# Performance work log

Hardware: AMD Instinct MI355X
Metric: run time of the kernel (lower is better)

The kernel has to match this reference:

```python
import jax, jax.numpy as jnp
import numpy as np
import math

# dims
C2, C1, T = 32, 64, 2048      # x shape
AVGF = 32                     # num_submatrices
SEG = T // AVGF               # 64
M = C1 * C2                   # M_size1 = 2048
TK = 3                        # num_blocks
HA = 16                       # num_heads
DH = M // HA                  # 128
EPS = 1e-5


def setup_inputs() -> dict:
    key = jax.random.key(0)
    ks = jax.random.split(key, 12)
    sc = 0.02  # scale params to keep fp32 activations finite
    return {
        "x": jax.random.normal(ks[0], (C2, C1, T), dtype=jnp.float32),
        "weight": jax.random.normal(ks[1], (M, M), dtype=jnp.float32) * sc,
        "Wqkv": jax.random.normal(ks[2], (TK, 3, HA, DH, M), dtype=jnp.float32) * sc,
        "Wo": jax.random.normal(ks[3], (TK, M, M), dtype=jnp.float32) * sc,
        "ln1_g": jnp.ones((M,), jnp.float32),
        "ln1_b": jnp.zeros((M,), jnp.float32),
        "ln2_g": jnp.ones((M,), jnp.float32),
        "ln2_b": jnp.zeros((M,), jnp.float32),
        "fc1_w": jax.random.normal(ks[4], (4 * M, M), dtype=jnp.float32) * sc,
        "fc1_b": jnp.zeros((4 * M,), jnp.float32),
        "fc2_w": jax.random.normal(ks[5], (M, 4 * M), dtype=jnp.float32) * sc,
        "fc2_b": jnp.zeros((M,), jnp.float32),
    }


def _ln(x, g, b):
    mu = jnp.mean(x, axis=-1, keepdims=True)
    var = jnp.var(x, axis=-1, keepdims=True)
    return (x - mu) / jnp.sqrt(var + EPS) * g + b


def _sinusoidal_bias():
    # bias[i, 2j]   = sin(i / 10000**(2*(2j)/M))  -- exponent uses even column index
    # bias[i, 2j+1] = cos(same angle)
    i = jnp.arange(AVGF, dtype=jnp.float32)[:, None]          # [avgf, 1]
    j = jnp.arange(0, M, 2, dtype=jnp.float32)[None, :]       # [1, M/2] even cols
    ang = i / jnp.power(10000.0, 2.0 * j / M)                 # [avgf, M/2]
    return jnp.stack([jnp.sin(ang), jnp.cos(ang)], axis=-1).reshape(AVGF, M)


def reference(x, weight, Wqkv, Wo, ln1_g, ln1_b, ln2_g, ln2_b,
              fc1_w, fc1_b, fc2_w, fc2_b):
    inp = jnp.transpose(x, (2, 1, 0))                          # [T, C1, C2]
    # segment-average over time -> [avgf, C1, C2]
    inputc = inp.reshape(AVGF, SEG, C1, C2).mean(axis=1)
    altx = inputc.reshape(AVGF, M)                             # [avgf, M]
    s = jnp.einsum('lm,im->il', weight, altx)                  # [avgf, M]
    s = s + _sinusoidal_bias()
    inv_sqrt_dh = 1.0 / math.sqrt(DH)
    for a in range(TK):                                        # fixed small block loop
        y = _ln(s, ln1_g, ln1_b)
        qkv = jnp.einsum('xhdm,im->xihd', Wqkv[a], y)          # [3, avgf, hA, Dh]
        q, k, v = qkv[0], qkv[1], qkv[2]
        rsa = jnp.einsum('ihd,ihd->ih', q * inv_sqrt_dh, k)    # per-token scalar attn
        imv = jnp.cumsum(rsa[..., None] * v, axis=0)           # serial inter-block scan
        s = jnp.einsum('nm,im->in', Wo[a], imv.reshape(AVGF, M)) + s
        s = _ln(s, ln2_g, ln2_b) + s
        h = jax.nn.gelu(s @ fc1_w.T + fc1_b, approximate=False)
        s = h @ fc2_w.T + fc2_b
    return s.reshape(AVGF, C1, C2)
```

## Files before the change

kernel.cpp:

```cpp
#include <hip/hip_runtime.h>
#include <math.h>

typedef __attribute__((ext_vector_type(4))) float f32x4;
typedef __attribute__((ext_vector_type(8))) short bf16x8;

__device__ inline short f2bf(float f) {
    union { float f; unsigned u; } v; v.f = f;
    unsigned u = v.u;
    u += 0x7fffu + ((u >> 16) & 1u);
    return (short)(u >> 16);
}

__global__ __launch_bounds__(256) void k_avg_init(const float* __restrict__ x,
                                                  float* __restrict__ altx,
                                                  float* __restrict__ s) {
    int blk = blockIdx.x, t = threadIdx.x;
    if (blk < 512) {
        int wv = t >> 6, lane = t & 63;
        int p = blk * 4 + wv;
        const float* row = x + (size_t)p * 2048;
        int c2 = p >> 6, c1 = p & 63;
        int m = c1 * 32 + c2;
        for (int seg = 0; seg < 32; ++seg) {
            float v = row[seg * 64 + lane];
            for (int off = 32; off; off >>= 1) v += __shfl_xor(v, off, 64);
            if (lane == 0) altx[seg * 2048 + m] = v * (1.0f / 64.0f);
        }
    } else {
        int i = blk - 512;
        const float kln = logf(10000.0f) / 1024.0f;
        for (int l = t; l < 2048; l += 256) {
            int c = l & ~1;
            float ang = (float)i * expf(-(float)c * kln);
            s[i * 2048 + l] = (l & 1) ? cosf(ang) : sinf(ang);
        }
    }
}

__device__ inline void row_stats(const float* __restrict__ row, float& mu, float& rstd) {
    float sm = 0.f, ss = 0.f;
    for (int idx = threadIdx.x; idx < 2048; idx += 256) {
        float v = row[idx]; sm += v; ss += v * v;
    }
    for (int off = 32; off; off >>= 1) {
        sm += __shfl_xor(sm, off, 64);
        ss += __shfl_xor(ss, off, 64);
    }
    __shared__ float as[4], bs[4];
    int wv = threadIdx.x >> 6, lane = threadIdx.x & 63;
    if (lane == 0) { as[wv] = sm; bs[wv] = ss; }
    __syncthreads();
    sm = as[0] + as[1] + as[2] + as[3];
    ss = bs[0] + bs[1] + bs[2] + bs[3];
    mu = sm * (1.0f / 2048.0f);
    float var = ss * (1.0f / 2048.0f) - mu * mu;
    rstd = rsqrtf(var + 1e-5f);
}

__global__ __launch_bounds__(256) void k_prep1(const float* __restrict__ s,
                                               const float* __restrict__ g,
                                               const float* __restrict__ b,
                                               float* __restrict__ y,
                                               float* __restrict__ s2,
                                               float* __restrict__ qkv) {
    int blk = blockIdx.x;
    if (blk < 32) {
        const float* row = s + blk * 2048;
        float mu, rstd; row_stats(row, mu, rstd);
        float* yr = y + blk * 2048;
        float* cr = s2 + blk * 2048;
        for (int idx = threadIdx.x; idx < 2048; idx += 256) {
            float v = row[idx];
            yr[idx] = (v - mu) * rstd * g[idx] + b[idx];
            cr[idx] = v;
        }
    } else {
        int z = blk - 32;
        float4* p4 = (float4*)(qkv + (size_t)z * 8192);
        float4 zero = {0.f, 0.f, 0.f, 0.f};
        for (int idx = threadIdx.x; idx < 2048; idx += 256) p4[idx] = zero;
    }
}

__global__ __launch_bounds__(256) void k_scan(const float* __restrict__ qkv,
                                              float* __restrict__ imv) {
    int h = blockIdx.x, t = threadIdx.x;
    __shared__ float rsa[32];
    if (t < 32) {
        const float* qr = qkv + (size_t)t * 6144 + h * 128;
        const float* kr = qr + 2048;
        float acc = 0.f;
        for (int d = 0; d < 128; ++d) acc += qr[d] * kr[d];
        rsa[t] = acc * 0.08838834764831845f;
    }
    __syncthreads();
    if (t < 128) {
        float acc = 0.f;
        for (int i = 0; i < 32; ++i) {
            acc += rsa[i] * qkv[(size_t)i * 6144 + 4096 + h * 128 + t];
            imv[i * 2048 + h * 128 + t] = acc;
        }
    }
}

__global__ __launch_bounds__(256) void k_prep2(const float* __restrict__ s2,
                                               const float* __restrict__ g,
                                               const float* __restrict__ b,
                                               float* __restrict__ sout,
                                               float* __restrict__ h) {
    int blk = blockIdx.x;
    if (blk < 32) {
        const float* row = s2 + blk * 2048;
        float mu, rstd; row_stats(row, mu, rstd);
        float* sr = sout + blk * 2048;
        for (int idx = threadIdx.x; idx < 2048; idx += 256) {
            float v = row[idx];
            sr[idx] = (v - mu) * rstd * g[idx] + b[idx] + v;
        }
    } else {
        int z = blk - 32;
        float4* p4 = (float4*)(h + (size_t)z * 8192);
        float4 zero = {0.f, 0.f, 0.f, 0.f};
        for (int idx = threadIdx.x; idx < 2048; idx += 256) p4[idx] = zero;
    }
}

__global__ __launch_bounds__(256) void k_act(float* __restrict__ h,
                                             const float* __restrict__ fc1_b,
                                             float* __restrict__ sout,
                                             const float* __restrict__ fc2_b) {
    int blk = blockIdx.x, t = threadIdx.x;
    if (blk < 128) {
        size_t base = ((size_t)blk * 256 + t) * 8;
        #pragma unroll
        for (int j = 0; j < 8; ++j) {
            size_t idx = base + j;
            float v = h[idx] + fc1_b[idx & 8191];
            h[idx] = 0.5f * v * (1.0f + erff(v * 0.70710678118654752f));
        }
    } else {
        size_t base = ((size_t)(blk - 128) * 256 + t) * 8;
        #pragma unroll
        for (int j = 0; j < 8; ++j) {
            size_t idx = base + j;
            sout[idx] = fc2_b[idx & 2047];
        }
    }
}

template<int TAG>
__global__ __launch_bounds__(256, 4) void k_gemm(const float* __restrict__ W,
                                                 const float* __restrict__ act,
                                                 float* __restrict__ out,
                                                 int N, int K) {
    constexpr int KC = 128;
    constexpr int S = KC / 32;
    __shared__ short lAs[32][KC + 8];
    int t = threadIdx.x;
    int lane = t & 63, wv = t >> 6;
    int m = lane & 15, q = lane >> 4;
    int nb = blockIdx.x * 64 + wv * 16;
    size_t kbeg = (size_t)blockIdx.y * KC;

    constexpr int APT = KC / 8;
    int arow = t >> 3, acol = (t & 7) * APT;
    const float* ap = act + (size_t)arow * K + kbeg + acol;
    float4 areg[APT / 4];
    #pragma unroll
    for (int j = 0; j < APT / 4; ++j) areg[j] = *(const float4*)(ap + j * 4);

    const float* B = W + (size_t)(nb + m) * K + kbeg + q * 8;
    float4 Bb[2 * S];
    #pragma unroll
    for (int s = 0; s < S; ++s) {
        Bb[2 * s]     = *(const float4*)(B + s * 32);
        Bb[2 * s + 1] = *(const float4*)(B + s * 32 + 4);
    }

    #pragma unroll
    for (int j = 0; j < APT / 4; ++j) {
        short4 c = { f2bf(areg[j].x), f2bf(areg[j].y), f2bf(areg[j].z), f2bf(areg[j].w) };
        *(short4*)&lAs[arow][acol + j * 4] = c;
    }
    __syncthreads();

    f32x4 acc0 = {0.f,0.f,0.f,0.f};
    f32x4 acc1 = {0.f,0.f,0.f,0.f};
    #pragma unroll
    for (int s = 0; s < S; ++s) {
        bf16x8 fa0 = *(const bf16x8*)&lAs[m][s * 32 + q * 8];
        bf16x8 fa1 = *(const bf16x8*)&lAs[m + 16][s * 32 + q * 8];
        float4 bl = Bb[2 * s], bh = Bb[2 * s + 1];
        bf16x8 fb = { f2bf(bl.x), f2bf(bl.y), f2bf(bl.z), f2bf(bl.w),
                      f2bf(bh.x), f2bf(bh.y), f2bf(bh.z), f2bf(bh.w) };
        acc0 = __builtin_amdgcn_mfma_f32_16x16x32_bf16(fa0, fb, acc0, 0, 0, 0);
        acc1 = __builtin_amdgcn_mfma_f32_16x16x32_bf16(fa1, fb, acc1, 0, 0, 0);
    }

    float* op = out + (size_t)(q * 4) * N + nb + m;
    #pragma unroll
    for (int r = 0; r < 4; ++r) {
        atomicAdd(op + (size_t)r * N, acc0[r]);
        atomicAdd(op + (size_t)(r + 16) * N, acc1[r]);
    }
}

extern "C" void kernel_launch(void* const* d_in, const int* in_sizes, int n_in,
                              void* d_out, int out_size, void* d_ws, size_t ws_size,
                              hipStream_t stream) {
    const float* x      = (const float*)d_in[0];
    const float* weight = (const float*)d_in[1];
    const float* Wqkv   = (const float*)d_in[2];
    const float* Wo     = (const float*)d_in[3];
    const float* ln1_g  = (const float*)d_in[4];
    const float* ln1_b  = (const float*)d_in[5];
    const float* ln2_g  = (const float*)d_in[6];
    const float* ln2_b  = (const float*)d_in[7];
    const float* fc1_w  = (const float*)d_in[8];
    const float* fc1_b  = (const float*)d_in[9];
    const float* fc2_w  = (const float*)d_in[10];
    const float* fc2_b  = (const float*)d_in[11];
    float* ws   = (float*)d_ws;
    float* altx = ws;
    float* sbuf = ws + 65536;
    float* y    = ws + 131072;
    float* s2   = ws + 196608;
    float* imv  = ws + 262144;
    float* qkv  = ws + 327680;
    float* h    = ws + 524288;
    float* outF = (float*)d_out;

    k_avg_init<<<544, 256, 0, stream>>>(x, altx, sbuf);
    k_gemm<0><<<dim3(32, 16), 256, 0, stream>>>(weight, altx, sbuf, 2048, 2048);
    for (int a = 0; a < 3; ++a) {
        k_prep1<<<56, 256, 0, stream>>>(sbuf, ln1_g, ln1_b, y, s2, qkv);
        k_gemm<1><<<dim3(96, 16), 256, 0, stream>>>(Wqkv + (size_t)a * 12582912, y, qkv, 6144, 2048);
        k_scan<<<16, 256, 0, stream>>>(qkv, imv);
        k_gemm<2><<<dim3(32, 16), 256, 0, stream>>>(Wo + (size_t)a * 4194304, imv, s2, 2048, 2048);
        k_prep2<<<64, 256, 0, stream>>>(s2, ln2_g, ln2_b, sbuf, h);
        k_gemm<3><<<dim3(128, 16), 256, 0, stream>>>(fc1_w, sbuf, h, 8192, 2048);
        float* sout = (a == 2) ? outF : sbuf;
        k_act<<<160, 256, 0, stream>>>(h, fc1_b, sout, fc2_b);
        k_gemm<4><<<dim3(32, 64), 256, 0, stream>>>(fc2_w, h, sout, 2048, 8192);
    }
}
```

Measured before the change: 552.5 us.

## Replace atomic split-K accumulation with partial buffers reduced in consumer kernels

The GEMM kernel now writes per-split partial results to a scratch pool with plain stores instead of atomicAdd. Downstream kernels (layernorm, scan, GELU, final output) sum the partials, so the separate zeroing and bias-init passes disappear. Each block also covers a larger K range (256 or 512) and double-buffers its weight register loads, which means fewer splits and less partial traffic. The costs are extra scratch memory, partial-sum reads in every consumer, and higher register use, reflected in the lower launch-bounds occupancy hint.

```diff
diff --git a/kernel.cpp b/kernel.cpp
--- a/kernel.cpp
+++ b/kernel.cpp
@@ -13,7 +13,7 @@
 
 __global__ __launch_bounds__(256) void k_avg_init(const float* __restrict__ x,
                                                   float* __restrict__ altx,
-                                                  float* __restrict__ s) {
+                                                  float* __restrict__ bias0) {
     int blk = blockIdx.x, t = threadIdx.x;
     if (blk < 512) {
         int wv = t >> 6, lane = t & 63;
@@ -32,176 +32,215 @@
         for (int l = t; l < 2048; l += 256) {
             int c = l & ~1;
             float ang = (float)i * expf(-(float)c * kln);
-            s[i * 2048 + l] = (l & 1) ? cosf(ang) : sinf(ang);
-        }
-    }
-}
-
-__device__ inline void row_stats(const float* __restrict__ row, float& mu, float& rstd) {
-    float sm = 0.f, ss = 0.f;
-    for (int idx = threadIdx.x; idx < 2048; idx += 256) {
-        float v = row[idx]; sm += v; ss += v * v;
-    }
-    for (int off = 32; off; off >>= 1) {
-        sm += __shfl_xor(sm, off, 64);
-        ss += __shfl_xor(ss, off, 64);
-    }
-    __shared__ float as[4], bs[4];
-    int wv = threadIdx.x >> 6, lane = threadIdx.x & 63;
-    if (lane == 0) { as[wv] = sm; bs[wv] = ss; }
-    __syncthreads();
-    sm = as[0] + as[1] + as[2] + as[3];
-    ss = bs[0] + bs[1] + bs[2] + bs[3];
-    mu = sm * (1.0f / 2048.0f);
-    float var = ss * (1.0f / 2048.0f) - mu * mu;
-    rstd = rsqrtf(var + 1e-5f);
-}
-
-__global__ __launch_bounds__(256) void k_prep1(const float* __restrict__ s,
-                                               const float* __restrict__ g,
-                                               const float* __restrict__ b,
-                                               float* __restrict__ y,
-                                               float* __restrict__ s2,
-                                               float* __restrict__ qkv) {
-    int blk = blockIdx.x;
-    if (blk < 32) {
-        const float* row = s + blk * 2048;
-        float mu, rstd; row_stats(row, mu, rstd);
-        float* yr = y + blk * 2048;
-        float* cr = s2 + blk * 2048;
-        for (int idx = threadIdx.x; idx < 2048; idx += 256) {
-            float v = row[idx];
-            yr[idx] = (v - mu) * rstd * g[idx] + b[idx];
-            cr[idx] = v;
-        }
-    } else {
-        int z = blk - 32;
-        float4* p4 = (float4*)(qkv + (size_t)z * 8192);
-        float4 zero = {0.f, 0.f, 0.f, 0.f};
-        for (int idx = threadIdx.x; idx < 2048; idx += 256) p4[idx] = zero;
-    }
-}
-
-__global__ __launch_bounds__(256) void k_scan(const float* __restrict__ qkv,
-                                              float* __restrict__ imv) {
-    int h = blockIdx.x, t = threadIdx.x;
-    __shared__ float rsa[32];
-    if (t < 32) {
-        const float* qr = qkv + (size_t)t * 6144 + h * 128;
-        const float* kr = qr + 2048;
-        float acc = 0.f;
-        for (int d = 0; d < 128; ++d) acc += qr[d] * kr[d];
-        rsa[t] = acc * 0.08838834764831845f;
-    }
-    __syncthreads();
-    if (t < 128) {
-        float acc = 0.f;
-        for (int i = 0; i < 32; ++i) {
-            acc += rsa[i] * qkv[(size_t)i * 6144 + 4096 + h * 128 + t];
-            imv[i * 2048 + h * 128 + t] = acc;
-        }
-    }
-}
-
-__global__ __launch_bounds__(256) void k_prep2(const float* __restrict__ s2,
-                                               const float* __restrict__ g,
-                                               const float* __restrict__ b,
-                                               float* __restrict__ sout,
-                                               float* __restrict__ h) {
-    int blk = blockIdx.x;
-    if (blk < 32) {
-        const float* row = s2 + blk * 2048;
-        float mu, rstd; row_stats(row, mu, rstd);
-        float* sr = sout + blk * 2048;
-        for (int idx = threadIdx.x; idx < 2048; idx += 256) {
-            float v = row[idx];
-            sr[idx] = (v - mu) * rstd * g[idx] + b[idx] + v;
-        }
-    } else {
-        int z = blk - 32;
-        float4* p4 = (float4*)(h + (size_t)z * 8192);
-        float4 zero = {0.f, 0.f, 0.f, 0.f};
-        for (int idx = threadIdx.x; idx < 2048; idx += 256) p4[idx] = zero;
-    }
-}
-
-__global__ __launch_bounds__(256) void k_act(float* __restrict__ h,
-                                             const float* __restrict__ fc1_b,
-                                             float* __restrict__ sout,
-                                             const float* __restrict__ fc2_b) {
-    int blk = blockIdx.x, t = threadIdx.x;
-    if (blk < 128) {
-        size_t base = ((size_t)blk * 256 + t) * 8;
-        #pragma unroll
-        for (int j = 0; j < 8; ++j) {
-            size_t idx = base + j;
-            float v = h[idx] + fc1_b[idx & 8191];
-            h[idx] = 0.5f * v * (1.0f + erff(v * 0.70710678118654752f));
-        }
-    } else {
-        size_t base = ((size_t)(blk - 128) * 256 + t) * 8;
-        #pragma unroll
-        for (int j = 0; j < 8; ++j) {
-            size_t idx = base + j;
-            sout[idx] = fc2_b[idx & 2047];
-        }
-    }
-}
-
-template<int TAG>
-__global__ __launch_bounds__(256, 4) void k_gemm(const float* __restrict__ W,
+            bias0[i * 2048 + l] = (l & 1) ? cosf(ang) : sinf(ang);
+        }
+    }
+}
+
+template<int KR>
+__global__ __launch_bounds__(256, 3) void k_gemm(const float* __restrict__ W,
                                                  const float* __restrict__ act,
-                                                 float* __restrict__ out,
+                                                 float* __restrict__ part,
                                                  int N, int K) {
-    constexpr int KC = 128;
-    constexpr int S = KC / 32;
-    __shared__ short lAs[32][KC + 8];
+    constexpr int NKC = KR / 128;
+    __shared__ short lAs[32][KR + 8];
     int t = threadIdx.x;
     int lane = t & 63, wv = t >> 6;
     int m = lane & 15, q = lane >> 4;
     int nb = blockIdx.x * 64 + wv * 16;
-    size_t kbeg = (size_t)blockIdx.y * KC;
-
-    constexpr int APT = KC / 8;
+    size_t kbeg = (size_t)blockIdx.y * KR;
+
+    constexpr int APT = KR / 8;
     int arow = t >> 3, acol = (t & 7) * APT;
     const float* ap = act + (size_t)arow * K + kbeg + acol;
     float4 areg[APT / 4];
     #pragma unroll
     for (int j = 0; j < APT / 4; ++j) areg[j] = *(const float4*)(ap + j * 4);
-
-    const float* B = W + (size_t)(nb + m) * K + kbeg + q * 8;
-    float4 Bb[2 * S];
-    #pragma unroll
-    for (int s = 0; s < S; ++s) {
-        Bb[2 * s]     = *(const float4*)(B + s * 32);
-        Bb[2 * s + 1] = *(const float4*)(B + s * 32 + 4);
-    }
-
     #pragma unroll
     for (int j = 0; j < APT / 4; ++j) {
         short4 c = { f2bf(areg[j].x), f2bf(areg[j].y), f2bf(areg[j].z), f2bf(areg[j].w) };
         *(short4*)&lAs[arow][acol + j * 4] = c;
     }
-    __syncthreads();
-
-    f32x4 acc0 = {0.f,0.f,0.f,0.f};
-    f32x4 acc1 = {0.f,0.f,0.f,0.f};
-    #pragma unroll
-    for (int s = 0; s < S; ++s) {
-        bf16x8 fa0 = *(const bf16x8*)&lAs[m][s * 32 + q * 8];
-        bf16x8 fa1 = *(const bf16x8*)&lAs[m + 16][s * 32 + q * 8];
-        float4 bl = Bb[2 * s], bh = Bb[2 * s + 1];
-        bf16x8 fb = { f2bf(bl.x), f2bf(bl.y), f2bf(bl.z), f2bf(bl.w),
-                      f2bf(bh.x), f2bf(bh.y), f2bf(bh.z), f2bf(bh.w) };
-        acc0 = __builtin_amdgcn_mfma_f32_16x16x32_bf16(fa0, fb, acc0, 0, 0, 0);
-        acc1 = __builtin_amdgcn_mfma_f32_16x16x32_bf16(fa1, fb, acc1, 0, 0, 0);
-    }
-
-    float* op = out + (size_t)(q * 4) * N + nb + m;
+
+    const float* B = W + (size_t)(nb + m) * K + kbeg + q * 8;
+    float4 Bb[2][8];
+    #pragma unroll
+    for (int s = 0; s < 4; ++s) {
+        Bb[0][2 * s]     = *(const float4*)(B + s * 32);
+        Bb[0][2 * s + 1] = *(const float4*)(B + s * 32 + 4);
+    }
+    __syncthreads();
+
+    f32x4 acc0 = {0.f, 0.f, 0.f, 0.f};
+    f32x4 acc1 = {0.f, 0.f, 0.f, 0.f};
+    #pragma unroll
+    for (int kc = 0; kc < NKC; ++kc) {
+        const int cur = kc & 1;
+        if (kc + 1 < NKC) {
+            const float* Bn = B + (kc + 1) * 128;
+            #pragma unroll
+            for (int s = 0; s < 4; ++s) {
+                Bb[cur ^ 1][2 * s]     = *(const float4*)(Bn + s * 32);
+                Bb[cur ^ 1][2 * s + 1] = *(const float4*)(Bn + s * 32 + 4);
+            }
+        }
+        #pragma unroll
+        for (int s = 0; s < 4; ++s) {
+            bf16x8 fa0 = *(const bf16x8*)&lAs[m][kc * 128 + s * 32 + q * 8];
+            bf16x8 fa1 = *(const bf16x8*)&lAs[m + 16][kc * 128 + s * 32 + q * 8];
+            float4 bl = Bb[cur][2 * s], bh = Bb[cur][2 * s + 1];
+            bf16x8 fb = { f2bf(bl.x), f2bf(bl.y), f2bf(bl.z), f2bf(bl.w),
+                          f2bf(bh.x), f2bf(bh.y), f2bf(bh.z), f2bf(bh.w) };
+            acc0 = __builtin_amdgcn_mfma_f32_16x16x32_bf16(fa0, fb, acc0, 0, 0, 0);
+            acc1 = __builtin_amdgcn_mfma_f32_16x16x32_bf16(fa1, fb, acc1, 0, 0, 0);
+        }
+    }
+
+    float* op = part + (size_t)blockIdx.y * 32 * N + (size_t)(q * 4) * N + nb + m;
     #pragma unroll
     for (int r = 0; r < 4; ++r) {
-        atomicAdd(op + (size_t)r * N, acc0[r]);
-        atomicAdd(op + (size_t)(r + 16) * N, acc1[r]);
+        op[(size_t)r * N] = acc0[r];
+        op[(size_t)(r + 16) * N] = acc1[r];
+    }
+}
+
+template<bool FINAL>
+__global__ __launch_bounds__(256) void k_prep1(const float* __restrict__ part, int nsplit,
+                                               const float* __restrict__ base2d,
+                                               const float* __restrict__ bias1d,
+                                               const float* __restrict__ g,
+                                               const float* __restrict__ b,
+                                               float* __restrict__ sres,
+                                               float* __restrict__ y) {
+    int row = blockIdx.x, t = threadIdx.x;
+    float v[8];
+    const float* p0 = part + row * 2048;
+    #pragma unroll
+    for (int j = 0; j < 8; ++j) {
+        int col = j * 256 + t;
+        float acc = base2d ? base2d[row * 2048 + col] : bias1d[col];
+        const float* p = p0 + col;
+        for (int s = 0; s < nsplit; ++s) acc += p[(size_t)s * 65536];
+        v[j] = acc;
+    }
+    float* sr = sres + row * 2048;
+    if (FINAL) {
+        #pragma unroll
+        for (int j = 0; j < 8; ++j) sr[j * 256 + t] = v[j];
+        return;
+    }
+    float sm = 0.f, ss = 0.f;
+    #pragma unroll
+    for (int j = 0; j < 8; ++j) { sm += v[j]; ss += v[j] * v[j]; }
+    for (int off = 32; off; off >>= 1) { sm += __shfl_xor(sm, off, 64); ss += __shfl_xor(ss, off, 64); }
+    __shared__ float as[4], bs[4];
+    int wv = t >> 6, lane = t & 63;
+    if (lane == 0) { as[wv] = sm; bs[wv] = ss; }
+    __syncthreads();
+    sm = as[0] + as[1] + as[2] + as[3];
+    ss = bs[0] + bs[1] + bs[2] + bs[3];
+    float mu = sm * (1.0f / 2048.0f);
+    float rstd = rsqrtf(ss * (1.0f / 2048.0f) - mu * mu + 1e-5f);
+    float* yr = y + row * 2048;
+    #pragma unroll
+    for (int j = 0; j < 8; ++j) {
+        int col = j * 256 + t;
+        sr[col] = v[j];
+        yr[col] = (v[j] - mu) * rstd * g[col] + b[col];
+    }
+}
+
+__global__ __launch_bounds__(256) void k_prep2(const float* __restrict__ part,
+                                               const float* __restrict__ sin_,
+                                               const float* __restrict__ g,
+                                               const float* __restrict__ b,
+                                               float* __restrict__ sout) {
+    int row = blockIdx.x, t = threadIdx.x;
+    float v[8];
+    const float* p0 = part + row * 2048;
+    #pragma unroll
+    for (int j = 0; j < 8; ++j) {
+        int col = j * 256 + t;
+        float acc = sin_[row * 2048 + col];
+        const float* p = p0 + col;
+        #pragma unroll
+        for (int s = 0; s < 8; ++s) acc += p[(size_t)s * 65536];
+        v[j] = acc;
+    }
+    float sm = 0.f, ss = 0.f;
+    #pragma unroll
+    for (int j = 0; j < 8; ++j) { sm += v[j]; ss += v[j] * v[j]; }
+    for (int off = 32; off; off >>= 1) { sm += __shfl_xor(sm, off, 64); ss += __shfl_xor(ss, off, 64); }
+    __shared__ float as[4], bs[4];
+    int wv = t >> 6, lane = t & 63;
+    if (lane == 0) { as[wv] = sm; bs[wv] = ss; }
+    __syncthreads();
+    sm = as[0] + as[1] + as[2] + as[3];
+    ss = bs[0] + bs[1] + bs[2] + bs[3];
+    float mu = sm * (1.0f / 2048.0f);
+    float rstd = rsqrtf(ss * (1.0f / 2048.0f) - mu * mu + 1e-5f);
+    float* sr = sout + row * 2048;
+    #pragma unroll
+    for (int j = 0; j < 8; ++j) {
+        int col = j * 256 + t;
+        sr[col] = (v[j] - mu) * rstd * g[col] + b[col] + v[j];
+    }
+}
+
+__global__ __launch_bounds__(256) void k_scan(const float* __restrict__ part,
+                                              float* __restrict__ imv) {
+    int h = blockIdx.x, t = threadIdx.x;
+    __shared__ float vq[32][129], vk[32][129], vv[32][129];
+    __shared__ float rsa[32];
+    #pragma unroll
+    for (int kk = 0; kk < 16; ++kk) {
+        int flat = kk * 256 + t;
+        int i = flat >> 7, d = flat & 127;
+        const float* p = part + (size_t)i * 6144 + h * 128 + d;
+        float aq = 0.f, ak = 0.f, av = 0.f;
+        #pragma unroll
+        for (int s = 0; s < 8; ++s) {
+            const float* ps = p + (size_t)s * 196608;
+            aq += ps[0]; ak += ps[2048]; av += ps[4096];
+        }
+        vq[i][d] = aq; vk[i][d] = ak; vv[i][d] = av;
+    }
+    __syncthreads();
+    {
+        int i = t >> 3, sub = t & 7;
+        float acc = 0.f;
+        #pragma unroll
+        for (int dd = 0; dd < 16; ++dd) {
+            int d = sub * 16 + dd;
+            acc += vq[i][d] * vk[i][d];
+        }
+        acc += __shfl_xor(acc, 1, 64);
+        acc += __shfl_xor(acc, 2, 64);
+        acc += __shfl_xor(acc, 4, 64);
+        if (sub == 0) rsa[i] = acc * 0.08838834764831845f;
+    }
+    __syncthreads();
+    if (t < 128) {
+        float acc = 0.f;
+        #pragma unroll
+        for (int i = 0; i < 32; ++i) {
+            acc += rsa[i] * vv[i][t];
+            imv[i * 2048 + h * 128 + t] = acc;
+        }
+    }
+}
+
+__global__ __launch_bounds__(256) void k_act(const float* __restrict__ part,
+                                             const float* __restrict__ fc1_b,
+                                             float* __restrict__ h) {
+    int idx0 = blockIdx.x * 2048 + threadIdx.x;
+    #pragma unroll
+    for (int j = 0; j < 8; ++j) {
+        int idx = idx0 + j * 256;
+        float v = fc1_b[idx & 8191];
+        #pragma unroll
+        for (int s = 0; s < 4; ++s) v += part[(size_t)s * 262144 + idx];
+        h[idx] = 0.5f * v * (1.0f + erff(v * 0.70710678118654752f));
     }
 }
 
@@ -220,27 +259,32 @@
     const float* fc1_b  = (const float*)d_in[9];
     const float* fc2_w  = (const float*)d_in[10];
     const float* fc2_b  = (const float*)d_in[11];
-    float* ws   = (float*)d_ws;
-    float* altx = ws;
-    float* sbuf = ws + 65536;
-    float* y    = ws + 131072;
-    float* s2   = ws + 196608;
-    float* imv  = ws + 262144;
-    float* qkv  = ws + 327680;
-    float* h    = ws + 524288;
-    float* outF = (float*)d_out;
-
-    k_avg_init<<<544, 256, 0, stream>>>(x, altx, sbuf);
-    k_gemm<0><<<dim3(32, 16), 256, 0, stream>>>(weight, altx, sbuf, 2048, 2048);
+    float* ws    = (float*)d_ws;
+    float* altx  = ws;
+    float* bias0 = ws + 65536;
+    float* sres  = ws + 131072;
+    float* y     = ws + 196608;
+    float* imv   = ws + 262144;
+    float* h     = ws + 327680;
+    float* part2 = ws + 589824;
+    float* pool  = ws + 1114112;
+    float* outF  = (float*)d_out;
+
+    k_avg_init<<<544, 256, 0, stream>>>(x, altx, bias0);
+    k_gemm<256><<<dim3(32, 8), 256, 0, stream>>>(weight, altx, pool, 2048, 2048);
     for (int a = 0; a < 3; ++a) {
-        k_prep1<<<56, 256, 0, stream>>>(sbuf, ln1_g, ln1_b, y, s2, qkv);
-        k_gemm<1><<<dim3(96, 16), 256, 0, stream>>>(Wqkv + (size_t)a * 12582912, y, qkv, 6144, 2048);
-        k_scan<<<16, 256, 0, stream>>>(qkv, imv);
-        k_gemm<2><<<dim3(32, 16), 256, 0, stream>>>(Wo + (size_t)a * 4194304, imv, s2, 2048, 2048);
-        k_prep2<<<64, 256, 0, stream>>>(s2, ln2_g, ln2_b, sbuf, h);
-        k_gemm<3><<<dim3(128, 16), 256, 0, stream>>>(fc1_w, sbuf, h, 8192, 2048);
-        float* sout = (a == 2) ? outF : sbuf;
-        k_act<<<160, 256, 0, stream>>>(h, fc1_b, sout, fc2_b);
-        k_gemm<4><<<dim3(32, 64), 256, 0, stream>>>(fc2_w, h, sout, 2048, 8192);
-    }
-}
+        k_prep1<false><<<32, 256, 0, stream>>>(pool, a ? 16 : 8,
+                                               a ? nullptr : bias0,
+                                               a ? fc2_b : nullptr,
+                                               ln1_g, ln1_b, sres, y);
+        k_gemm<256><<<dim3(96, 8), 256, 0, stream>>>(Wqkv + (size_t)a * 12582912, y, pool, 6144, 2048);
+        k_scan<<<16, 256, 0, stream>>>(pool, imv);
+        k_gemm<256><<<dim3(32, 8), 256, 0, stream>>>(Wo + (size_t)a * 4194304, imv, part2, 2048, 2048);
+        k_prep2<<<32, 256, 0, stream>>>(part2, sres, ln2_g, ln2_b, sres);
+        k_gemm<512><<<dim3(128, 4), 256, 0, stream>>>(fc1_w, sres, pool, 8192, 2048);
+        k_act<<<128, 256, 0, stream>>>(pool, fc1_b, h);
+        k_gemm<512><<<dim3(32, 16), 256, 0, stream>>>(fc2_w, h, pool, 2048, 8192);
+    }
+    k_prep1<true><<<32, 256, 0, stream>>>(pool, 16, nullptr, fc2_b,
+                                          nullptr, nullptr, outF, nullptr);
+}
```

Measured after the change: 648.1 us. +17.3%, slower.

## Fuse all stages into one persistent megakernel with grid-wide barriers

Applied to the files above, without the earlier changes.

Replaces the sequence of about two dozen kernel launches with a single persistent kernel of 512 blocks. The blocks step through each stage (averaging, layer norms, GEMMs, scan, GELU) and separate them with an atomic-counter grid barrier. GEMM tiles are handed out as a strided task loop over the fixed block count, and the scan's q·k dot product is split across 8 threads per token. The aim is to remove launch overhead and inter-kernel gaps. In exchange, GEMMs run at most 2 blocks per CU instead of 4, each barrier spins on a global atomic, and correctness depends on all 512 blocks being resident at once.

```diff
diff --git a/kernel.cpp b/kernel.cpp
--- a/kernel.cpp
+++ b/kernel.cpp
@@ -11,14 +11,136 @@
     return (short)(u >> 16);
 }
 
-__global__ __launch_bounds__(256) void k_avg_init(const float* __restrict__ x,
-                                                  float* __restrict__ altx,
-                                                  float* __restrict__ s) {
-    int blk = blockIdx.x, t = threadIdx.x;
-    if (blk < 512) {
+struct Params {
+    const float *x, *weight, *Wqkv, *Wo, *ln1_g, *ln1_b, *ln2_g, *ln2_b,
+                *fc1_w, *fc1_b, *fc2_w, *fc2_b;
+    float *ws, *out;
+    unsigned *bar;
+};
+
+#define NBLK 512u
+
+__device__ inline void gsync(unsigned* bar, unsigned target) {
+    __syncthreads();
+    if (threadIdx.x == 0) {
+        __threadfence();
+        __hip_atomic_fetch_add(bar, 1u, __ATOMIC_RELAXED, __HIP_MEMORY_SCOPE_AGENT);
+        while (__hip_atomic_load(bar, __ATOMIC_RELAXED, __HIP_MEMORY_SCOPE_AGENT) < target)
+            __builtin_amdgcn_s_sleep(1);
+        __threadfence();
+    }
+    __syncthreads();
+}
+
+__device__ inline void gemm_tasks(const float* __restrict__ W, const float* __restrict__ act,
+                                  float* __restrict__ out, int N, int K,
+                                  short lAs[32][136], int bid, int t) {
+    int nbx = N >> 6;
+    int ntask = nbx * (K >> 7);
+    int lane = t & 63, wv = t >> 6, m = lane & 15, q = lane >> 4;
+    int arow = t >> 3, acol = (t & 7) * 16;
+    for (int task = bid; task < ntask; task += NBLK) {
+        int bx = task % nbx, by = task / nbx;
+        size_t kbeg = (size_t)by << 7;
+        int nb = bx * 64 + wv * 16;
+        const float* ap = act + (size_t)arow * K + kbeg + acol;
+        float4 a0 = *(const float4*)(ap);
+        float4 a1 = *(const float4*)(ap + 4);
+        float4 a2 = *(const float4*)(ap + 8);
+        float4 a3 = *(const float4*)(ap + 12);
+        const float* B = W + (size_t)(nb + m) * K + kbeg + q * 8;
+        float4 Bb[8];
+        #pragma unroll
+        for (int s = 0; s < 4; ++s) {
+            Bb[2 * s]     = *(const float4*)(B + s * 32);
+            Bb[2 * s + 1] = *(const float4*)(B + s * 32 + 4);
+        }
+        __syncthreads();
+        {
+            short4 c0 = { f2bf(a0.x), f2bf(a0.y), f2bf(a0.z), f2bf(a0.w) };
+            short4 c1 = { f2bf(a1.x), f2bf(a1.y), f2bf(a1.z), f2bf(a1.w) };
+            short4 c2 = { f2bf(a2.x), f2bf(a2.y), f2bf(a2.z), f2bf(a2.w) };
+            short4 c3 = { f2bf(a3.x), f2bf(a3.y), f2bf(a3.z), f2bf(a3.w) };
+            *(short4*)&lAs[arow][acol]      = c0;
+            *(short4*)&lAs[arow][acol + 4]  = c1;
+            *(short4*)&lAs[arow][acol + 8]  = c2;
+            *(short4*)&lAs[arow][acol + 12] = c3;
+        }
+        __syncthreads();
+        f32x4 acc0 = {0.f, 0.f, 0.f, 0.f};
+        f32x4 acc1 = {0.f, 0.f, 0.f, 0.f};
+        #pragma unroll
+        for (int s = 0; s < 4; ++s) {
+            bf16x8 fa0 = *(const bf16x8*)&lAs[m][s * 32 + q * 8];
+            bf16x8 fa1 = *(const bf16x8*)&lAs[m + 16][s * 32 + q * 8];
+            float4 bl = Bb[2 * s], bh = Bb[2 * s + 1];
+            bf16x8 fb = { f2bf(bl.x), f2bf(bl.y), f2bf(bl.z), f2bf(bl.w),
+                          f2bf(bh.x), f2bf(bh.y), f2bf(bh.z), f2bf(bh.w) };
+            acc0 = __builtin_amdgcn_mfma_f32_16x16x32_bf16(fa0, fb, acc0, 0, 0, 0);
+            acc1 = __builtin_amdgcn_mfma_f32_16x16x32_bf16(fa1, fb, acc1, 0, 0, 0);
+        }
+        float* op = out + (size_t)(q * 4) * N + nb + m;
+        #pragma unroll
+        for (int r = 0; r < 4; ++r) {
+            atomicAdd(op + (size_t)r * N, acc0[r]);
+            atomicAdd(op + (size_t)(r + 16) * N, acc1[r]);
+        }
+    }
+}
+
+__device__ inline void ln_task(const float* __restrict__ row,
+                               const float* __restrict__ g, const float* __restrict__ b,
+                               float* __restrict__ outA, float* __restrict__ outB,
+                               float* red, int t) {
+    float v[8];
+    #pragma unroll
+    for (int j = 0; j < 8; ++j) v[j] = row[j * 256 + t];
+    float sm = 0.f, ss = 0.f;
+    #pragma unroll
+    for (int j = 0; j < 8; ++j) { sm += v[j]; ss += v[j] * v[j]; }
+    for (int off = 32; off; off >>= 1) { sm += __shfl_xor(sm, off, 64); ss += __shfl_xor(ss, off, 64); }
+    int wv = t >> 6, lane = t & 63;
+    if (lane == 0) { red[wv] = sm; red[4 + wv] = ss; }
+    __syncthreads();
+    sm = red[0] + red[1] + red[2] + red[3];
+    ss = red[4] + red[5] + red[6] + red[7];
+    float mu = sm * (1.0f / 2048.0f);
+    float rstd = rsqrtf(ss * (1.0f / 2048.0f) - mu * mu + 1e-5f);
+    #pragma unroll
+    for (int j = 0; j < 8; ++j) {
+        int col = j * 256 + t;
+        float lnv = (v[j] - mu) * rstd * g[col] + b[col];
+        if (outB) { outA[col] = lnv; outB[col] = v[j]; }
+        else      { outA[col] = lnv + v[j]; }
+    }
+}
+
+__device__ inline void zero_task(float* __restrict__ p, int t) {
+    float4 z = {0.f, 0.f, 0.f, 0.f};
+    float4* p4 = (float4*)p;
+    #pragma unroll
+    for (int k = 0; k < 8; ++k) p4[k * 256 + t] = z;
+}
+
+__global__ __launch_bounds__(256, 2) void k_mega(Params P) {
+    __shared__ short lAs[32][136];
+    __shared__ float red[8];
+    __shared__ float rsa[32];
+    int bid = blockIdx.x, t = threadIdx.x;
+    unsigned ph = 0;
+
+    float* altx = P.ws;
+    float* sbuf = P.ws + 65536;
+    float* y    = P.ws + 131072;
+    float* s2   = P.ws + 196608;
+    float* imv  = P.ws + 262144;
+    float* qkv  = P.ws + 327680;
+    float* h    = P.ws + 524288;
+
+    {
         int wv = t >> 6, lane = t & 63;
-        int p = blk * 4 + wv;
-        const float* row = x + (size_t)p * 2048;
+        int p = bid * 4 + wv;
+        const float* row = P.x + (size_t)p * 2048;
         int c2 = p >> 6, c1 = p & 63;
         int m = c1 * 32 + c2;
         for (int seg = 0; seg < 32; ++seg) {
@@ -26,221 +148,102 @@
             for (int off = 32; off; off >>= 1) v += __shfl_xor(v, off, 64);
             if (lane == 0) altx[seg * 2048 + m] = v * (1.0f / 64.0f);
         }
-    } else {
-        int i = blk - 512;
-        const float kln = logf(10000.0f) / 1024.0f;
-        for (int l = t; l < 2048; l += 256) {
-            int c = l & ~1;
-            float ang = (float)i * expf(-(float)c * kln);
-            s[i * 2048 + l] = (l & 1) ? cosf(ang) : sinf(ang);
-        }
-    }
-}
-
-__device__ inline void row_stats(const float* __restrict__ row, float& mu, float& rstd) {
-    float sm = 0.f, ss = 0.f;
-    for (int idx = threadIdx.x; idx < 2048; idx += 256) {
-        float v = row[idx]; sm += v; ss += v * v;
-    }
-    for (int off = 32; off; off >>= 1) {
-        sm += __shfl_xor(sm, off, 64);
-        ss += __shfl_xor(ss, off, 64);
-    }
-    __shared__ float as[4], bs[4];
-    int wv = threadIdx.x >> 6, lane = threadIdx.x & 63;
-    if (lane == 0) { as[wv] = sm; bs[wv] = ss; }
-    __syncthreads();
-    sm = as[0] + as[1] + as[2] + as[3];
-    ss = bs[0] + bs[1] + bs[2] + bs[3];
-    mu = sm * (1.0f / 2048.0f);
-    float var = ss * (1.0f / 2048.0f) - mu * mu;
-    rstd = rsqrtf(var + 1e-5f);
-}
-
-__global__ __launch_bounds__(256) void k_prep1(const float* __restrict__ s,
-                                               const float* __restrict__ g,
-                                               const float* __restrict__ b,
-                                               float* __restrict__ y,
-                                               float* __restrict__ s2,
-                                               float* __restrict__ qkv) {
-    int blk = blockIdx.x;
-    if (blk < 32) {
-        const float* row = s + blk * 2048;
-        float mu, rstd; row_stats(row, mu, rstd);
-        float* yr = y + blk * 2048;
-        float* cr = s2 + blk * 2048;
-        for (int idx = threadIdx.x; idx < 2048; idx += 256) {
-            float v = row[idx];
-            yr[idx] = (v - mu) * rstd * g[idx] + b[idx];
-            cr[idx] = v;
-        }
-    } else {
-        int z = blk - 32;
-        float4* p4 = (float4*)(qkv + (size_t)z * 8192);
-        float4 zero = {0.f, 0.f, 0.f, 0.f};
-        for (int idx = threadIdx.x; idx < 2048; idx += 256) p4[idx] = zero;
-    }
-}
-
-__global__ __launch_bounds__(256) void k_scan(const float* __restrict__ qkv,
-                                              float* __restrict__ imv) {
-    int h = blockIdx.x, t = threadIdx.x;
-    __shared__ float rsa[32];
-    if (t < 32) {
-        const float* qr = qkv + (size_t)t * 6144 + h * 128;
-        const float* kr = qr + 2048;
-        float acc = 0.f;
-        for (int d = 0; d < 128; ++d) acc += qr[d] * kr[d];
-        rsa[t] = acc * 0.08838834764831845f;
-    }
-    __syncthreads();
-    if (t < 128) {
-        float acc = 0.f;
-        for (int i = 0; i < 32; ++i) {
-            acc += rsa[i] * qkv[(size_t)i * 6144 + 4096 + h * 128 + t];
-            imv[i * 2048 + h * 128 + t] = acc;
-        }
-    }
-}
-
-__global__ __launch_bounds__(256) void k_prep2(const float* __restrict__ s2,
-                                               const float* __restrict__ g,
-                                               const float* __restrict__ b,
-                                               float* __restrict__ sout,
-                                               float* __restrict__ h) {
-    int blk = blockIdx.x;
-    if (blk < 32) {
-        const float* row = s2 + blk * 2048;
-        float mu, rstd; row_stats(row, mu, rstd);
-        float* sr = sout + blk * 2048;
-        for (int idx = threadIdx.x; idx < 2048; idx += 256) {
-            float v = row[idx];
-            sr[idx] = (v - mu) * rstd * g[idx] + b[idx] + v;
-        }
-    } else {
-        int z = blk - 32;
-        float4* p4 = (float4*)(h + (size_t)z * 8192);
-        float4 zero = {0.f, 0.f, 0.f, 0.f};
-        for (int idx = threadIdx.x; idx < 2048; idx += 256) p4[idx] = zero;
-    }
-}
-
-__global__ __launch_bounds__(256) void k_act(float* __restrict__ h,
-                                             const float* __restrict__ fc1_b,
-                                             float* __restrict__ sout,
-                                             const float* __restrict__ fc2_b) {
-    int blk = blockIdx.x, t = threadIdx.x;
-    if (blk < 128) {
-        size_t base = ((size_t)blk * 256 + t) * 8;
-        #pragma unroll
-        for (int j = 0; j < 8; ++j) {
-            size_t idx = base + j;
-            float v = h[idx] + fc1_b[idx & 8191];
-            h[idx] = 0.5f * v * (1.0f + erff(v * 0.70710678118654752f));
-        }
-    } else {
-        size_t base = ((size_t)(blk - 128) * 256 + t) * 8;
-        #pragma unroll
-        for (int j = 0; j < 8; ++j) {
-            size_t idx = base + j;
-            sout[idx] = fc2_b[idx & 2047];
-        }
-    }
-}
-
-template<int TAG>
-__global__ __launch_bounds__(256, 4) void k_gemm(const float* __restrict__ W,
-                                                 const float* __restrict__ act,
-                                                 float* __restrict__ out,
-                                                 int N, int K) {
-    constexpr int KC = 128;
-    constexpr int S = KC / 32;
-    __shared__ short lAs[32][KC + 8];
-    int t = threadIdx.x;
-    int lane = t & 63, wv = t >> 6;
-    int m = lane & 15, q = lane >> 4;
-    int nb = blockIdx.x * 64 + wv * 16;
-    size_t kbeg = (size_t)blockIdx.y * KC;
-
-    constexpr int APT = KC / 8;
-    int arow = t >> 3, acol = (t & 7) * APT;
-    const float* ap = act + (size_t)arow * K + kbeg + acol;
-    float4 areg[APT / 4];
-    #pragma unroll
-    for (int j = 0; j < APT / 4; ++j) areg[j] = *(const float4*)(ap + j * 4);
-
-    const float* B = W + (size_t)(nb + m) * K + kbeg + q * 8;
-    float4 Bb[2 * S];
-    #pragma unroll
-    for (int s = 0; s < S; ++s) {
-        Bb[2 * s]     = *(const float4*)(B + s * 32);
-        Bb[2 * s + 1] = *(const float4*)(B + s * 32 + 4);
-    }
-
-    #pragma unroll
-    for (int j = 0; j < APT / 4; ++j) {
-        short4 c = { f2bf(areg[j].x), f2bf(areg[j].y), f2bf(areg[j].z), f2bf(areg[j].w) };
-        *(short4*)&lAs[arow][acol + j * 4] = c;
-    }
-    __syncthreads();
-
-    f32x4 acc0 = {0.f,0.f,0.f,0.f};
-    f32x4 acc1 = {0.f,0.f,0.f,0.f};
-    #pragma unroll
-    for (int s = 0; s < S; ++s) {
-        bf16x8 fa0 = *(const bf16x8*)&lAs[m][s * 32 + q * 8];
-        bf16x8 fa1 = *(const bf16x8*)&lAs[m + 16][s * 32 + q * 8];
-        float4 bl = Bb[2 * s], bh = Bb[2 * s + 1];
-        bf16x8 fb = { f2bf(bl.x), f2bf(bl.y), f2bf(bl.z), f2bf(bl.w),
-                      f2bf(bh.x), f2bf(bh.y), f2bf(bh.z), f2bf(bh.w) };
-        acc0 = __builtin_amdgcn_mfma_f32_16x16x32_bf16(fa0, fb, acc0, 0, 0, 0);
-        acc1 = __builtin_amdgcn_mfma_f32_16x16x32_bf16(fa1, fb, acc1, 0, 0, 0);
-    }
-
-    float* op = out + (size_t)(q * 4) * N + nb + m;
-    #pragma unroll
-    for (int r = 0; r < 4; ++r) {
-        atomicAdd(op + (size_t)r * N, acc0[r]);
-        atomicAdd(op + (size_t)(r + 16) * N, acc1[r]);
+        if (bid < 32) {
+            const float kln = logf(10000.0f) / 1024.0f;
+            for (int l = t; l < 2048; l += 256) {
+                int c = l & ~1;
+                float ang = (float)bid * expf(-(float)c * kln);
+                sbuf[bid * 2048 + l] = (l & 1) ? cosf(ang) : sinf(ang);
+            }
+        }
+    }
+    gsync(P.bar, ++ph * NBLK);
+    gemm_tasks(P.weight, altx, sbuf, 2048, 2048, lAs, bid, t);
+
+    for (int a = 0; a < 3; ++a) {
+        gsync(P.bar, ++ph * NBLK);
+        if (bid < 32)      ln_task(sbuf + bid * 2048, P.ln1_g, P.ln1_b,
+                                   y + bid * 2048, s2 + bid * 2048, red, t);
+        else if (bid < 56) zero_task(qkv + (size_t)(bid - 32) * 8192, t);
+        gsync(P.bar, ++ph * NBLK);
+        gemm_tasks(P.Wqkv + (size_t)a * 12582912, y, qkv, 6144, 2048, lAs, bid, t);
+        gsync(P.bar, ++ph * NBLK);
+        if (bid < 16) {
+            int hh = bid;
+            int i = t >> 3, sub = t & 7;
+            const float* qr = qkv + (size_t)i * 6144 + hh * 128 + sub * 16;
+            const float* kr = qr + 2048;
+            float acc = 0.f;
+            #pragma unroll
+            for (int dd = 0; dd < 16; ++dd) acc += qr[dd] * kr[dd];
+            acc += __shfl_xor(acc, 1, 64);
+            acc += __shfl_xor(acc, 2, 64);
+            acc += __shfl_xor(acc, 4, 64);
+            if (sub == 0) rsa[i] = acc * 0.08838834764831845f;
+            __syncthreads();
+            if (t < 128) {
+                float vs[32];
+                #pragma unroll
+                for (int i2 = 0; i2 < 32; ++i2)
+                    vs[i2] = qkv[(size_t)i2 * 6144 + 4096 + hh * 128 + t];
+                float a2 = 0.f;
+                #pragma unroll
+                for (int i2 = 0; i2 < 32; ++i2) {
+                    a2 += rsa[i2] * vs[i2];
+                    imv[i2 * 2048 + hh * 128 + t] = a2;
+                }
+            }
+        }
+        gsync(P.bar, ++ph * NBLK);
+        gemm_tasks(P.Wo + (size_t)a * 4194304, imv, s2, 2048, 2048, lAs, bid, t);
+        gsync(P.bar, ++ph * NBLK);
+        if (bid < 32)      ln_task(s2 + bid * 2048, P.ln2_g, P.ln2_b,
+                                   sbuf + bid * 2048, nullptr, red, t);
+        else if (bid < 64) zero_task(h + (size_t)(bid - 32) * 8192, t);
+        gsync(P.bar, ++ph * NBLK);
+        gemm_tasks(P.fc1_w, sbuf, h, 8192, 2048, lAs, bid, t);
+        gsync(P.bar, ++ph * NBLK);
+        float* sout = (a == 2) ? P.out : sbuf;
+        if (bid < 128) {
+            size_t base = ((size_t)bid * 256 + t) * 8;
+            #pragma unroll
+            for (int j = 0; j < 8; ++j) {
+                size_t idx = base + j;
+                float v = h[idx] + P.fc1_b[idx & 8191];
+                h[idx] = 0.5f * v * (1.0f + erff(v * 0.70710678118654752f));
+            }
+        } else if (bid < 160) {
+            size_t base = ((size_t)(bid - 128) * 256 + t) * 8;
+            #pragma unroll
+            for (int j = 0; j < 8; ++j) {
+                size_t idx = base + j;
+                sout[idx] = P.fc2_b[idx & 2047];
+            }
+        }
+        gsync(P.bar, ++ph * NBLK);
+        gemm_tasks(P.fc2_w, h, sout, 2048, 8192, lAs, bid, t);
     }
 }
 
 extern "C" void kernel_launch(void* const* d_in, const int* in_sizes, int n_in,
                               void* d_out, int out_size, void* d_ws, size_t ws_size,
                               hipStream_t stream) {
-    const float* x      = (const float*)d_in[0];
-    const float* weight = (const float*)d_in[1];
-    const float* Wqkv   = (const float*)d_in[2];
-    const float* Wo     = (const float*)d_in[3];
-    const float* ln1_g  = (const float*)d_in[4];
-    const float* ln1_b  = (const float*)d_in[5];
-    const float* ln2_g  = (const float*)d_in[6];
-    const float* ln2_b  = (const float*)d_in[7];
-    const float* fc1_w  = (const float*)d_in[8];
-    const float* fc1_b  = (const float*)d_in[9];
-    const float* fc2_w  = (const float*)d_in[10];
-    const float* fc2_b  = (const float*)d_in[11];
-    float* ws   = (float*)d_ws;
-    float* altx = ws;
-    float* sbuf = ws + 65536;
-    float* y    = ws + 131072;
-    float* s2   = ws + 196608;
-    float* imv  = ws + 262144;
-    float* qkv  = ws + 327680;
-    float* h    = ws + 524288;
-    float* outF = (float*)d_out;
-
-    k_avg_init<<<544, 256, 0, stream>>>(x, altx, sbuf);
-    k_gemm<0><<<dim3(32, 16), 256, 0, stream>>>(weight, altx, sbuf, 2048, 2048);
-    for (int a = 0; a < 3; ++a) {
-        k_prep1<<<56, 256, 0, stream>>>(sbuf, ln1_g, ln1_b, y, s2, qkv);
-        k_gemm<1><<<dim3(96, 16), 256, 0, stream>>>(Wqkv + (size_t)a * 12582912, y, qkv, 6144, 2048);
-        k_scan<<<16, 256, 0, stream>>>(qkv, imv);
-        k_gemm<2><<<dim3(32, 16), 256, 0, stream>>>(Wo + (size_t)a * 4194304, imv, s2, 2048, 2048);
-        k_prep2<<<64, 256, 0, stream>>>(s2, ln2_g, ln2_b, sbuf, h);
-        k_gemm<3><<<dim3(128, 16), 256, 0, stream>>>(fc1_w, sbuf, h, 8192, 2048);
-        float* sout = (a == 2) ? outF : sbuf;
-        k_act<<<160, 256, 0, stream>>>(h, fc1_b, sout, fc2_b);
-        k_gemm<4><<<dim3(32, 64), 256, 0, stream>>>(fc2_w, h, sout, 2048, 8192);
-    }
-}
+    Params P;
+    P.x      = (const float*)d_in[0];
+    P.weight = (const float*)d_in[1];
+    P.Wqkv   = (const float*)d_in[2];
+    P.Wo     = (const float*)d_in[3];
+    P.ln1_g  = (const float*)d_in[4];
+    P.ln1_b  = (const float*)d_in[5];
+    P.ln2_g  = (const float*)d_in[6];
+    P.ln2_b  = (const float*)d_in[7];
+    P.fc1_w  = (const float*)d_in[8];
+    P.fc1_b  = (const float*)d_in[9];
+    P.fc2_w  = (const float*)d_in[10];
+    P.fc2_b  = (const float*)d_in[11];
+    P.ws     = (float*)d_ws;
+    P.out    = (float*)d_out;
+    P.bar    = (unsigned*)((float*)d_ws + (1 << 20));
+    hipMemsetAsync(P.bar, 0, 64, stream);
+    k_mega<<<NBLK, 256, 0, stream>>>(P);
+}
```

Result: slower. 1.736 ms (+214.3%).
